# Kernel tuning notes

Hardware: AMD Instinct MI355X
Metric: run time of the kernel (lower is better)

Reference implementation:

```python
import jax, jax.numpy as jnp
import numpy as np

G = 20000      # num genes in table
D = 128        # per-pathway embedding dim
P = 32         # num pathways (n_nmf_embedding)
H = 128        # item_hidden_size
B = 4096       # num combos (segments)
S = 8192       # gathered rows (2 genes per combo)
G_OUT = 20000  # output_dimension
TEMP = 1.0     # softmax_temperature


def setup_inputs() -> dict:
    key = jax.random.key(0)
    ks = jax.random.split(key, 9)
    gene_embeddings = jax.random.normal(ks[0], (G, D, P), dtype=jnp.float32)
    # normalize by median norm as in __init__
    norms = jnp.linalg.norm(gene_embeddings, axis=1, keepdims=True)  # [G,1,P]
    med = jnp.median(norms)
    gene_embeddings = gene_embeddings / jnp.where(med == 0, 1.0, med)
    W1 = jax.random.normal(ks[1], (D, H), dtype=jnp.float32) * (1.0 / np.sqrt(D))
    b1 = jnp.zeros((H,), dtype=jnp.float32)
    W2 = jax.random.normal(ks[2], (H, H), dtype=jnp.float32) * (1.0 / np.sqrt(H))
    b2 = jnp.zeros((H,), dtype=jnp.float32)
    pw = jax.random.normal(ks[3], (P,), dtype=jnp.float32)  # pathway pooling logits
    Wout = jax.random.normal(ks[4], (H, G_OUT), dtype=jnp.float32) * (1.0 / np.sqrt(H))
    bout = jnp.zeros((G_OUT,), dtype=jnp.float32)
    locs_gene = jax.random.randint(ks[5], (S,), 0, G, dtype=jnp.int32)
    # each combo has 2 genes; segment ids cover 0..B-1 (torch.unique relabels to arange)
    locs_combos = jnp.repeat(jnp.arange(B, dtype=jnp.int32), S // B)
    return {
        "gene_embeddings": gene_embeddings, "W1": W1, "b1": b1, "W2": W2,
        "b2": b2, "pw": pw, "Wout": Wout, "bout": bout,
        "locs_gene": locs_gene, "locs_combos": locs_combos,
    }


def reference(gene_embeddings, W1, b1, W2, b2, pw, Wout, bout, locs_gene, locs_combos):
    # mask over the whole table, then gather rows (matches self.mask[locs_gene])
    mask_tab = (jnp.sum(gene_embeddings, axis=1, keepdims=True) != 0)  # [G,1,P]
    emb = gene_embeddings[locs_gene]        # [S,D,P] gather
    mask = mask_tab[locs_gene]              # [S,1,P]
    # pathway_encoder: MLP over the D axis, shared across pathways
    h = jax.nn.leaky_relu(jnp.einsum('sdp,dh->shp', emb, W1) + b1[None, :, None])
    h = jnp.einsum('shp,hk->skp', h, W2) + b2[None, :, None]
    h = jax.nn.leaky_relu(h)                # activation after encoder  [S,H,P]
    # per-combo group sum (fused segment-sum instead of the Python loop)
    seg = jax.ops.segment_sum(h, locs_combos, num_segments=B)                        # [B,H,P]
    mseg = jax.ops.segment_sum(mask.astype(jnp.float32), locs_combos, num_segments=B)  # [B,1,P]
    m = mseg > 0                            # [B,1,P]
    # Pool: masked temperature softmax over pathways with learnable weights
    logits = pw / TEMP                      # [P]
    logits = jnp.where(m, logits[None, None, :], -1e9)
    w = jax.nn.softmax(logits, axis=-1)     # [B,1,P]
    pooled = jnp.sum(seg * w, axis=-1)      # [B,H]
    # item_net: H -> num_genes
    out = pooled @ Wout + bout              # [B,G_OUT]
    return out
```

## Files before the change

### kernel.cpp

```cpp
#include <hip/hip_runtime.h>
#include <hip/hip_bf16.h>

#define GENES 20000
#define DD    128
#define PP    32
#define HH    128
#define NB    4096
#define GOUT  20000
#define GPAD  20096
#define CPB   16

typedef __attribute__((ext_vector_type(8))) short bf16x8;
typedef __attribute__((ext_vector_type(4))) float f32x4;

__device__ __forceinline__ unsigned short f2bf(float f) {
    unsigned int u = __float_as_uint(f);
    unsigned int lsb = (u >> 16) & 1u;
    u += 0x7fffu + lsb;
    return (unsigned short)(u >> 16);
}
__device__ __forceinline__ float bf2f(unsigned short s) {
    return __uint_as_float(((unsigned int)s) << 16);
}

__device__ __forceinline__ int swz(int r, int c) {
    return r * 128 + (((c >> 3) ^ (r & 15)) << 3) + (c & 7);
}

__global__ void prep_weights(const float* __restrict__ W1, const float* __restrict__ W2,
                             unsigned short* __restrict__ w1t, unsigned short* __restrict__ w2t) {
    int idx = blockIdx.x * 512 + threadIdx.x;
#pragma unroll
    for (int k = 0; k < 2; ++k, idx += 256) {
        int d = idx >> 7, h = idx & 127;
        int off = swz(h, d);
        w1t[off] = f2bf(W1[idx]);
        w2t[off] = f2bf(W2[idx]);
    }
}

__global__ void prep_wout(const float* __restrict__ Wout, unsigned short* __restrict__ woutT) {
    int g = blockIdx.x * 256 + threadIdx.x;
    if (g >= GPAD) return;
    if (g < GOUT) {
        for (int d0 = 0; d0 < 128; d0 += 8) {
            unsigned short buf[8];
#pragma unroll
            for (int j = 0; j < 8; ++j) buf[j] = f2bf(Wout[(size_t)(d0 + j) * GOUT + g]);
            *reinterpret_cast<uint4*>(&woutT[(size_t)g * 128 + d0]) =
                *reinterpret_cast<const uint4*>(buf);
        }
    } else {
        uint4 z = {0u, 0u, 0u, 0u};
        for (int d0 = 0; d0 < 128; d0 += 8)
            *reinterpret_cast<uint4*>(&woutT[(size_t)g * 128 + d0]) = z;
    }
}

__global__ __launch_bounds__(512) void encoder_kernel(
    const float* __restrict__ gene, const float* __restrict__ b1g,
    const float* __restrict__ b2g, const float* __restrict__ pwg,
    const int* __restrict__ locs_gene, const int* __restrict__ locs_combos,
    const unsigned short* __restrict__ w1t, const unsigned short* __restrict__ w2t,
    unsigned short* __restrict__ poolbf)
{
    __shared__ __align__(16) unsigned short w1L[128 * 128];
    __shared__ __align__(16) unsigned short w2L[128 * 128];
    __shared__ __align__(16) unsigned short aBuf[2][64 * 128];
    __shared__ float wrow[64];
    __shared__ float pp[8][128];

    const int t = threadIdx.x;
    const int lane = t & 63, wv = t >> 6;
    const int nrow = lane & 15, kg = lane >> 4;
    const int mt = wv >> 1, nh = wv & 1;
    const int rA = mt * 16 + nrow;

    {
        const uint4* s1 = reinterpret_cast<const uint4*>(w1t);
        const uint4* s2 = reinterpret_cast<const uint4*>(w2t);
        uint4* d1 = reinterpret_cast<uint4*>(w1L);
        uint4* d2 = reinterpret_cast<uint4*>(w2L);
        for (int i = t; i < 2048; i += 512) { d1[i] = s1[i]; d2[i] = s2[i]; }
    }
    float b1r[4], b2r[4];
#pragma unroll
    for (int nt = 0; nt < 4; ++nt) {
        int c = nh * 64 + nt * 16 + nrow;
        b1r[nt] = b1g[c]; b2r[nt] = b2g[c];
    }
    const float pwl = pwg[lane & 31];

    const int sl = t >> 8;
    const int w8 = t & 255;
    const int d0 = (w8 >> 3) * 4;
    const int pq = w8 & 7;

    const int c0 = blockIdx.x * CPB;

    float4 pf[4];
    {
        int g0 = locs_gene[2 * c0], g1 = locs_gene[2 * c0 + 1];
        const float* src = gene + (size_t)(sl ? g1 : g0) * 4096;
#pragma unroll
        for (int i = 0; i < 4; ++i)
            pf[i] = *reinterpret_cast<const float4*>(&src[(d0 + i) * 32 + pq * 4]);
#pragma unroll
        for (int q = 0; q < 4; ++q) {
            int r = sl * 32 + pq * 4 + q;
            unsigned int lo = (unsigned int)f2bf((&pf[0].x)[q]) |
                              ((unsigned int)f2bf((&pf[1].x)[q]) << 16);
            unsigned int hi = (unsigned int)f2bf((&pf[2].x)[q]) |
                              ((unsigned int)f2bf((&pf[3].x)[q]) << 16);
            uint2 v2 = {lo, hi};
            *reinterpret_cast<uint2*>(
                &aBuf[0][r * 128 + (((d0 >> 3) ^ (r & 15)) << 3) + (d0 & 7)]) = v2;
        }
    }
    __syncthreads();

    int cur = 0;
    for (int j = 0; j < CPB; ++j) {
        const int c = c0 + j;
        if (j + 1 < CPB) {
            int g0 = locs_gene[2 * (c + 1)], g1 = locs_gene[2 * (c + 1) + 1];
            const float* src = gene + (size_t)(sl ? g1 : g0) * 4096;
#pragma unroll
            for (int i = 0; i < 4; ++i)
                pf[i] = *reinterpret_cast<const float4*>(&src[(d0 + i) * 32 + pq * 4]);
        }
        const unsigned short* A = aBuf[cur];
        unsigned short* Aw = aBuf[cur];

        if (wv == 0) {
            float cs = 0.f;
#pragma unroll
            for (int cch = 0; cch < 16; ++cch) {
                int phys = cch ^ (lane & 15);
                bf16x8 v = *reinterpret_cast<const bf16x8*>(&A[lane * 128 + phys * 8]);
#pragma unroll
                for (int q = 0; q < 8; ++q) cs += bf2f((unsigned short)v[q]);
            }
            float other = __shfl_down(cs, 32);
            bool m = (cs != 0.f) || (other != 0.f);
            float logit = m ? pwl : -1e9f;
            float mx = logit;
#pragma unroll
            for (int o = 16; o >= 1; o >>= 1) mx = fmaxf(mx, __shfl_xor(mx, o, 32));
            float e = __expf(logit - mx);
            float se = e;
#pragma unroll
            for (int o = 16; o >= 1; o >>= 1) se += __shfl_xor(se, o, 32);
            float w = e / se;
            if (lane < 32) { wrow[lane] = w; wrow[lane + 32] = w; }
        }

        bf16x8 afr[4];
#pragma unroll
        for (int ks = 0; ks < 4; ++ks) {
            int phys = (ks * 4 + kg) ^ (rA & 15);
            afr[ks] = *reinterpret_cast<const bf16x8*>(&A[rA * 128 + phys * 8]);
        }
        f32x4 acc1[4];
#pragma unroll
        for (int nt = 0; nt < 4; ++nt) {
            f32x4 acc = {0.f, 0.f, 0.f, 0.f};
            int n = nh * 64 + nt * 16 + nrow;
#pragma unroll
            for (int ks = 0; ks < 4; ++ks) {
                int phys = (ks * 4 + kg) ^ (n & 15);
                bf16x8 bfr = *reinterpret_cast<const bf16x8*>(&w1L[n * 128 + phys * 8]);
                acc = __builtin_amdgcn_mfma_f32_16x16x32_bf16(afr[ks], bfr, acc, 0, 0, 0);
            }
            acc1[nt] = acc;
        }
        __syncthreads();

#pragma unroll
        for (int nt = 0; nt < 4; ++nt) {
            int cc = nh * 64 + nt * 16 + nrow;
#pragma unroll
            for (int i = 0; i < 4; ++i) {
                int r = mt * 16 + kg * 4 + i;
                float x = acc1[nt][i] + b1r[nt];
                x = (x >= 0.f) ? x : 0.01f * x;
                Aw[swz(r, cc)] = f2bf(x);
            }
        }
        __syncthreads();

        bf16x8 afr2[4];
#pragma unroll
        for (int ks = 0; ks < 4; ++ks) {
            int phys = (ks * 4 + kg) ^ (rA & 15);
            afr2[ks] = *reinterpret_cast<const bf16x8*>(&A[rA * 128 + phys * 8]);
        }
        float wr[4];
#pragma unroll
        for (int i = 0; i < 4; ++i) wr[i] = wrow[mt * 16 + kg * 4 + i];
        float part[4];
#pragma unroll
        for (int nt = 0; nt < 4; ++nt) {
            f32x4 acc = {0.f, 0.f, 0.f, 0.f};
            int n = nh * 64 + nt * 16 + nrow;
#pragma unroll
            for (int ks = 0; ks < 4; ++ks) {
                int phys = (ks * 4 + kg) ^ (n & 15);
                bf16x8 bfr = *reinterpret_cast<const bf16x8*>(&w2L[n * 128 + phys * 8]);
                acc = __builtin_amdgcn_mfma_f32_16x16x32_bf16(afr2[ks], bfr, acc, 0, 0, 0);
            }
            float s = 0.f;
#pragma unroll
            for (int i = 0; i < 4; ++i) {
                float x = acc[i] + b2r[nt];
                x = (x >= 0.f) ? x : 0.01f * x;
                s += x * wr[i];
            }
            part[nt] = s;
        }
#pragma unroll
        for (int nt = 0; nt < 4; ++nt) {
            float v = part[nt];
            v += __shfl_xor(v, 16);
            v += __shfl_xor(v, 32);
            part[nt] = v;
        }
        if (lane < 16) {
#pragma unroll
            for (int nt = 0; nt < 4; ++nt) pp[wv][nh * 64 + nt * 16 + lane] = part[nt];
        }
        __syncthreads();

        if (t < 128) {
            int base = t >> 6;
            float s = pp[base][t] + pp[base + 2][t] + pp[base + 4][t] + pp[base + 6][t];
            int seg = locs_combos[2 * c];
            poolbf[(size_t)seg * 128 + t] = f2bf(s);
        }
        if (j + 1 < CPB) {
            unsigned short* B = aBuf[cur ^ 1];
#pragma unroll
            for (int q = 0; q < 4; ++q) {
                int r = sl * 32 + pq * 4 + q;
                unsigned int lo = (unsigned int)f2bf((&pf[0].x)[q]) |
                                  ((unsigned int)f2bf((&pf[1].x)[q]) << 16);
                unsigned int hi = (unsigned int)f2bf((&pf[2].x)[q]) |
                                  ((unsigned int)f2bf((&pf[3].x)[q]) << 16);
                uint2 v2 = {lo, hi};
                *reinterpret_cast<uint2*>(
                    &B[r * 128 + (((d0 >> 3) ^ (r & 15)) << 3) + (d0 & 7)]) = v2;
            }
            cur ^= 1;
        }
        __syncthreads();
    }
}

__global__ __launch_bounds__(256) void out_gemm(
    const unsigned short* __restrict__ poolbf, const unsigned short* __restrict__ woutT,
    const float* __restrict__ boutg, float* __restrict__ out)
{
    int t = threadIdx.x;
    int lane = t & 63, wv = t >> 6;
    int nb0 = blockIdx.x * 128;
    int mb0 = blockIdx.y * 128 + wv * 32;
    int nrow = lane & 15, kg = lane >> 4;

    bf16x8 afr[2][4];
#pragma unroll
    for (int mt = 0; mt < 2; ++mt) {
        int row = mb0 + mt * 16 + nrow;
#pragma unroll
        for (int ks = 0; ks < 4; ++ks)
            afr[mt][ks] = *reinterpret_cast<const bf16x8*>(
                &poolbf[(size_t)row * 128 + ks * 32 + kg * 8]);
    }
#pragma unroll
    for (int nt = 0; nt < 8; ++nt) {
        int n = nb0 + nt * 16 + nrow;
        f32x4 a0 = {0.f, 0.f, 0.f, 0.f}, a1 = {0.f, 0.f, 0.f, 0.f};
#pragma unroll
        for (int ks = 0; ks < 4; ++ks) {
            bf16x8 bfr = *reinterpret_cast<const bf16x8*>(
                &woutT[(size_t)n * 128 + ks * 32 + kg * 8]);
            a0 = __builtin_amdgcn_mfma_f32_16x16x32_bf16(afr[0][ks], bfr, a0, 0, 0, 0);
            a1 = __builtin_amdgcn_mfma_f32_16x16x32_bf16(afr[1][ks], bfr, a1, 0, 0, 0);
        }
        int col = nb0 + nt * 16 + nrow;
        if (col < GOUT) {
            float bias = boutg[col];
#pragma unroll
            for (int i = 0; i < 4; ++i) {
                int r0 = mb0 + kg * 4 + i;
                out[(size_t)r0 * GOUT + col] = a0[i] + bias;
                out[(size_t)(r0 + 16) * GOUT + col] = a1[i] + bias;
            }
        }
    }
}

extern "C" void kernel_launch(void* const* d_in, const int* in_sizes, int n_in,
                              void* d_out, int out_size, void* d_ws, size_t ws_size,
                              hipStream_t stream) {
    const float* gene  = (const float*)d_in[0];
    const float* W1    = (const float*)d_in[1];
    const float* b1    = (const float*)d_in[2];
    const float* W2    = (const float*)d_in[3];
    const float* b2    = (const float*)d_in[4];
    const float* pw    = (const float*)d_in[5];
    const float* Wout  = (const float*)d_in[6];
    const float* bout  = (const float*)d_in[7];
    const int* locs_gene   = (const int*)d_in[8];
    const int* locs_combos = (const int*)d_in[9];
    float* out = (float*)d_out;

    char* ws = (char*)d_ws;
    unsigned short* w1t    = (unsigned short*)(ws);
    unsigned short* w2t    = (unsigned short*)(ws + 32768);
    unsigned short* woutT  = (unsigned short*)(ws + 65536);
    unsigned short* poolbf = (unsigned short*)(ws + 65536 + (size_t)GPAD * 256);

    hipLaunchKernelGGL(prep_weights, dim3(32), dim3(256), 0, stream, W1, W2, w1t, w2t);
    hipLaunchKernelGGL(prep_wout, dim3((GPAD + 255) / 256), dim3(256), 0, stream, Wout, woutT);
    hipLaunchKernelGGL(encoder_kernel, dim3(NB / CPB), dim3(512), 0, stream,
                       gene, b1, b2, pw, locs_gene, locs_combos, w1t, w2t, poolbf);
    hipLaunchKernelGGL(out_gemm, dim3((GPAD / 128), 32), dim3(256), 0, stream,
                       poolbf, woutT, bout, out);
}
```

Before: 212.3 us.

## Keep encoder weights in registers, fuse mask sums into staging, remap GEMM tiles

The encoder now keeps the W1/W2 bf16 MFMA fragments in registers instead of copying both weight matrices into LDS. That frees 64KB of shared memory, and launch bounds now request two 512-thread blocks per CU. The per-pathway column sums used for the mask are computed during staging with shuffles, replacing a full LDS rescan by wave 0. Staging of the next combo moves earlier so one barrier can be dropped. The output GEMM uses a 1D grid remapped across 8 groups (likely XCD-aware) for better L2 locality. The risks are register pressure from the 32 weight fragments and a changed prep layout.

Measured after the change: 274.2 us. 29.2% more time.

```diff
diff --git a/kernel.cpp b/kernel.cpp
--- a/kernel.cpp
+++ b/kernel.cpp
@@ -19,9 +19,15 @@
     u += 0x7fffu + lsb;
     return (unsigned short)(u >> 16);
 }
-__device__ __forceinline__ float bf2f(unsigned short s) {
-    return __uint_as_float(((unsigned int)s) << 16);
-}
+__device__ __forceinline__ unsigned int f2bf2(float a, float b) {
+    return (unsigned int)f2bf(a) | ((unsigned int)f2bf(b) << 16);
+}
+
+#define BARRIER() do { \
+    asm volatile("s_waitcnt lgkmcnt(0)" ::: "memory"); \
+    __builtin_amdgcn_s_barrier(); \
+    asm volatile("" ::: "memory"); \
+} while (0)
 
 __device__ __forceinline__ int swz(int r, int c) {
     return r * 128 + (((c >> 3) ^ (r & 15)) << 3) + (c & 7);
@@ -29,13 +35,12 @@
 
 __global__ void prep_weights(const float* __restrict__ W1, const float* __restrict__ W2,
                              unsigned short* __restrict__ w1t, unsigned short* __restrict__ w2t) {
-    int idx = blockIdx.x * 512 + threadIdx.x;
-#pragma unroll
-    for (int k = 0; k < 2; ++k, idx += 256) {
-        int d = idx >> 7, h = idx & 127;
-        int off = swz(h, d);
-        w1t[off] = f2bf(W1[idx]);
-        w2t[off] = f2bf(W2[idx]);
+    int o = blockIdx.x * 512 + threadIdx.x;
+#pragma unroll
+    for (int k = 0; k < 2; ++k, o += 256) {
+        int h = o >> 7, d = o & 127;
+        w1t[o] = f2bf(W1[d * 128 + h]);
+        w2t[o] = f2bf(W2[d * 128 + h]);
     }
 }
 
@@ -57,16 +62,15 @@
     }
 }
 
-__global__ __launch_bounds__(512) void encoder_kernel(
+__global__ __launch_bounds__(512, 2) void encoder_kernel(
     const float* __restrict__ gene, const float* __restrict__ b1g,
     const float* __restrict__ b2g, const float* __restrict__ pwg,
     const int* __restrict__ locs_gene, const int* __restrict__ locs_combos,
     const unsigned short* __restrict__ w1t, const unsigned short* __restrict__ w2t,
     unsigned short* __restrict__ poolbf)
 {
-    __shared__ __align__(16) unsigned short w1L[128 * 128];
-    __shared__ __align__(16) unsigned short w2L[128 * 128];
     __shared__ __align__(16) unsigned short aBuf[2][64 * 128];
+    __shared__ float pcol[2][4][64];
     __shared__ float wrow[64];
     __shared__ float pp[8][128];
 
@@ -76,18 +80,21 @@
     const int mt = wv >> 1, nh = wv & 1;
     const int rA = mt * 16 + nrow;
 
-    {
-        const uint4* s1 = reinterpret_cast<const uint4*>(w1t);
-        const uint4* s2 = reinterpret_cast<const uint4*>(w2t);
-        uint4* d1 = reinterpret_cast<uint4*>(w1L);
-        uint4* d2 = reinterpret_cast<uint4*>(w2L);
-        for (int i = t; i < 2048; i += 512) { d1[i] = s1[i]; d2[i] = s2[i]; }
+    bf16x8 w1f[4][4], w2f[4][4];
+#pragma unroll
+    for (int nt = 0; nt < 4; ++nt) {
+        int n = nh * 64 + nt * 16 + nrow;
+#pragma unroll
+        for (int ks = 0; ks < 4; ++ks) {
+            w1f[nt][ks] = *reinterpret_cast<const bf16x8*>(&w1t[n * 128 + (ks * 4 + kg) * 8]);
+            w2f[nt][ks] = *reinterpret_cast<const bf16x8*>(&w2t[n * 128 + (ks * 4 + kg) * 8]);
+        }
     }
     float b1r[4], b2r[4];
 #pragma unroll
     for (int nt = 0; nt < 4; ++nt) {
-        int c = nh * 64 + nt * 16 + nrow;
-        b1r[nt] = b1g[c]; b2r[nt] = b2g[c];
+        int cc = nh * 64 + nt * 16 + nrow;
+        b1r[nt] = b1g[cc]; b2r[nt] = b2g[cc];
     }
     const float pwl = pwg[lane & 31];
 
@@ -95,52 +102,54 @@
     const int w8 = t & 255;
     const int d0 = (w8 >> 3) * 4;
     const int pq = w8 & 7;
-
     const int c0 = blockIdx.x * CPB;
 
     float4 pf[4];
-    {
-        int g0 = locs_gene[2 * c0], g1 = locs_gene[2 * c0 + 1];
-        const float* src = gene + (size_t)(sl ? g1 : g0) * 4096;
+    auto loadCombo = [&](int c) {
+        int gsel = locs_gene[2 * c + sl];
+        const float* src = gene + (size_t)gsel * 4096 + d0 * 32 + pq * 4;
 #pragma unroll
         for (int i = 0; i < 4; ++i)
-            pf[i] = *reinterpret_cast<const float4*>(&src[(d0 + i) * 32 + pq * 4]);
+            pf[i] = *reinterpret_cast<const float4*>(src + i * 32);
+    };
+    auto stageCombo = [&](int buf) {
+        float ps[4];
 #pragma unroll
         for (int q = 0; q < 4; ++q) {
+            float a0 = (&pf[0].x)[q], a1 = (&pf[1].x)[q];
+            float a2 = (&pf[2].x)[q], a3 = (&pf[3].x)[q];
+            ps[q] = (a0 + a1) + (a2 + a3);
+            uint2 v2;
+            v2.x = f2bf2(a0, a1);
+            v2.y = f2bf2(a2, a3);
             int r = sl * 32 + pq * 4 + q;
-            unsigned int lo = (unsigned int)f2bf((&pf[0].x)[q]) |
-                              ((unsigned int)f2bf((&pf[1].x)[q]) << 16);
-            unsigned int hi = (unsigned int)f2bf((&pf[2].x)[q]) |
-                              ((unsigned int)f2bf((&pf[3].x)[q]) << 16);
-            uint2 v2 = {lo, hi};
             *reinterpret_cast<uint2*>(
-                &aBuf[0][r * 128 + (((d0 >> 3) ^ (r & 15)) << 3) + (d0 & 7)]) = v2;
-        }
-    }
+                &aBuf[buf][r * 128 + (((d0 >> 3) ^ (r & 15)) << 3) + (d0 & 7)]) = v2;
+        }
+#pragma unroll
+        for (int o = 8; o <= 32; o <<= 1)
+#pragma unroll
+            for (int q = 0; q < 4; ++q) ps[q] += __shfl_xor(ps[q], o);
+        if (lane < 8) {
+#pragma unroll
+            for (int q = 0; q < 4; ++q)
+                pcol[buf][wv & 3][sl * 32 + pq * 4 + q] = ps[q];
+        }
+    };
+
+    loadCombo(c0);
+    stageCombo(0);
     __syncthreads();
 
     int cur = 0;
+#pragma unroll 1
     for (int j = 0; j < CPB; ++j) {
         const int c = c0 + j;
-        if (j + 1 < CPB) {
-            int g0 = locs_gene[2 * (c + 1)], g1 = locs_gene[2 * (c + 1) + 1];
-            const float* src = gene + (size_t)(sl ? g1 : g0) * 4096;
-#pragma unroll
-            for (int i = 0; i < 4; ++i)
-                pf[i] = *reinterpret_cast<const float4*>(&src[(d0 + i) * 32 + pq * 4]);
-        }
-        const unsigned short* A = aBuf[cur];
-        unsigned short* Aw = aBuf[cur];
+        if (j + 1 < CPB) loadCombo(c + 1);
 
         if (wv == 0) {
-            float cs = 0.f;
-#pragma unroll
-            for (int cch = 0; cch < 16; ++cch) {
-                int phys = cch ^ (lane & 15);
-                bf16x8 v = *reinterpret_cast<const bf16x8*>(&A[lane * 128 + phys * 8]);
-#pragma unroll
-                for (int q = 0; q < 8; ++q) cs += bf2f((unsigned short)v[q]);
-            }
+            float cs = pcol[cur][0][lane] + pcol[cur][1][lane]
+                     + pcol[cur][2][lane] + pcol[cur][3][lane];
             float other = __shfl_down(cs, 32);
             bool m = (cs != 0.f) || (other != 0.f);
             float logit = m ? pwl : -1e9f;
@@ -155,27 +164,24 @@
             if (lane < 32) { wrow[lane] = w; wrow[lane + 32] = w; }
         }
 
+        const unsigned short* A = aBuf[cur];
         bf16x8 afr[4];
 #pragma unroll
-        for (int ks = 0; ks < 4; ++ks) {
-            int phys = (ks * 4 + kg) ^ (rA & 15);
-            afr[ks] = *reinterpret_cast<const bf16x8*>(&A[rA * 128 + phys * 8]);
-        }
+        for (int ks = 0; ks < 4; ++ks)
+            afr[ks] = *reinterpret_cast<const bf16x8*>(
+                &A[rA * 128 + (((ks * 4 + kg) ^ nrow) << 3)]);
         f32x4 acc1[4];
 #pragma unroll
         for (int nt = 0; nt < 4; ++nt) {
             f32x4 acc = {0.f, 0.f, 0.f, 0.f};
-            int n = nh * 64 + nt * 16 + nrow;
-#pragma unroll
-            for (int ks = 0; ks < 4; ++ks) {
-                int phys = (ks * 4 + kg) ^ (n & 15);
-                bf16x8 bfr = *reinterpret_cast<const bf16x8*>(&w1L[n * 128 + phys * 8]);
-                acc = __builtin_amdgcn_mfma_f32_16x16x32_bf16(afr[ks], bfr, acc, 0, 0, 0);
-            }
+#pragma unroll
+            for (int ks = 0; ks < 4; ++ks)
+                acc = __builtin_amdgcn_mfma_f32_16x16x32_bf16(afr[ks], w1f[nt][ks], acc, 0, 0, 0);
             acc1[nt] = acc;
         }
-        __syncthreads();
-
+        BARRIER();
+
+        unsigned short* Aw = aBuf[cur];
 #pragma unroll
         for (int nt = 0; nt < 4; ++nt) {
             int cc = nh * 64 + nt * 16 + nrow;
@@ -187,14 +193,13 @@
                 Aw[swz(r, cc)] = f2bf(x);
             }
         }
-        __syncthreads();
+        BARRIER();
 
         bf16x8 afr2[4];
 #pragma unroll
-        for (int ks = 0; ks < 4; ++ks) {
-            int phys = (ks * 4 + kg) ^ (rA & 15);
-            afr2[ks] = *reinterpret_cast<const bf16x8*>(&A[rA * 128 + phys * 8]);
-        }
+        for (int ks = 0; ks < 4; ++ks)
+            afr2[ks] = *reinterpret_cast<const bf16x8*>(
+                &A[rA * 128 + (((ks * 4 + kg) ^ nrow) << 3)]);
         float wr[4];
 #pragma unroll
         for (int i = 0; i < 4; ++i) wr[i] = wrow[mt * 16 + kg * 4 + i];
@@ -202,22 +207,19 @@
 #pragma unroll
         for (int nt = 0; nt < 4; ++nt) {
             f32x4 acc = {0.f, 0.f, 0.f, 0.f};
-            int n = nh * 64 + nt * 16 + nrow;
-#pragma unroll
-            for (int ks = 0; ks < 4; ++ks) {
-                int phys = (ks * 4 + kg) ^ (n & 15);
-                bf16x8 bfr = *reinterpret_cast<const bf16x8*>(&w2L[n * 128 + phys * 8]);
-                acc = __builtin_amdgcn_mfma_f32_16x16x32_bf16(afr2[ks], bfr, acc, 0, 0, 0);
-            }
+#pragma unroll
+            for (int ks = 0; ks < 4; ++ks)
+                acc = __builtin_amdgcn_mfma_f32_16x16x32_bf16(afr2[ks], w2f[nt][ks], acc, 0, 0, 0);
             float s = 0.f;
 #pragma unroll
             for (int i = 0; i < 4; ++i) {
                 float x = acc[i] + b2r[nt];
                 x = (x >= 0.f) ? x : 0.01f * x;
-                s += x * wr[i];
+                s = fmaf(x, wr[i], s);
             }
             part[nt] = s;
         }
+        if (j + 1 < CPB) stageCombo(cur ^ 1);
 #pragma unroll
         for (int nt = 0; nt < 4; ++nt) {
             float v = part[nt];
@@ -229,7 +231,7 @@
 #pragma unroll
             for (int nt = 0; nt < 4; ++nt) pp[wv][nh * 64 + nt * 16 + lane] = part[nt];
         }
-        __syncthreads();
+        BARRIER();
 
         if (t < 128) {
             int base = t >> 6;
@@ -237,22 +239,7 @@
             int seg = locs_combos[2 * c];
             poolbf[(size_t)seg * 128 + t] = f2bf(s);
         }
-        if (j + 1 < CPB) {
-            unsigned short* B = aBuf[cur ^ 1];
-#pragma unroll
-            for (int q = 0; q < 4; ++q) {
-                int r = sl * 32 + pq * 4 + q;
-                unsigned int lo = (unsigned int)f2bf((&pf[0].x)[q]) |
-                                  ((unsigned int)f2bf((&pf[1].x)[q]) << 16);
-                unsigned int hi = (unsigned int)f2bf((&pf[2].x)[q]) |
-                                  ((unsigned int)f2bf((&pf[3].x)[q]) << 16);
-                uint2 v2 = {lo, hi};
-                *reinterpret_cast<uint2*>(
-                    &B[r * 128 + (((d0 >> 3) ^ (r & 15)) << 3) + (d0 & 7)]) = v2;
-            }
-            cur ^= 1;
-        }
-        __syncthreads();
+        if (j + 1 < CPB) cur ^= 1;
     }
 }
 
@@ -262,8 +249,11 @@
 {
     int t = threadIdx.x;
     int lane = t & 63, wv = t >> 6;
-    int nb0 = blockIdx.x * 128;
-    int mb0 = blockIdx.y * 128 + wv * 32;
+    int id = blockIdx.x;
+    int wk = (id & 7) * 628 + (id >> 3);
+    int bx = wk >> 5, by = wk & 31;
+    int nb0 = bx * 128;
+    int mb0 = by * 128 + wv * 32;
     int nrow = lane & 15, kg = lane >> 4;
 
     bf16x8 afr[2][4];
@@ -324,6 +314,6 @@
     hipLaunchKernelGGL(prep_wout, dim3((GPAD + 255) / 256), dim3(256), 0, stream, Wout, woutT);
     hipLaunchKernelGGL(encoder_kernel, dim3(NB / CPB), dim3(512), 0, stream,
                        gene, b1, b2, pw, locs_gene, locs_combos, w1t, w2t, poolbf);
-    hipLaunchKernelGGL(out_gemm, dim3((GPAD / 128), 32), dim3(256), 0, stream,
+    hipLaunchKernelGGL(out_gemm, dim3(8 * 628), dim3(256), 0, stream,
                        poolbf, woutT, bout, out);
 }
```
